# Kernel tuning notes

Measured on AMD Instinct MI355X. Metric: run time of the kernel, lower is better.

## Reference

```python
import jax, jax.numpy as jnp
import numpy as np

H = 16
HD = 128
ROPE_BASE = 10000.0

def _rope_cos_sin(T, dtype):
    inv_freq = 1.0 / (ROPE_BASE ** (jnp.arange(0, HD, 2, dtype=jnp.float32) / HD))  # [HD/2]
    pos = jnp.arange(T, dtype=jnp.float32)
    freqs = pos[:, None] * inv_freq[None, :]  # [T, HD/2]
    return jnp.cos(freqs).astype(dtype), jnp.sin(freqs).astype(dtype)

def _apply_rotary(x, cos, sin):
    # x: [B,H,T,HD]; cos/sin: [T,HD/2]
    x1, x2 = x[..., : HD // 2], x[..., HD // 2 :]
    c = cos[None, None, :, :]
    s = sin[None, None, :, :]
    return jnp.concatenate([x1 * c - x2 * s, x1 * s + x2 * c], axis=-1)

def setup_inputs() -> dict:
    key = jax.random.key(0)
    ks = jax.random.split(key, 5)
    B, T, D = 2, 2048, 2048
    x = jax.random.normal(ks[0], (B, T, D), dtype=jnp.float32)
    Wqkv = jax.random.normal(ks[1], (3 * D, D), dtype=jnp.float32) * (D ** -0.5)
    bqkv = jax.random.normal(ks[2], (3 * D,), dtype=jnp.float32) * 0.02
    Wo = jax.random.normal(ks[3], (D, D), dtype=jnp.float32) * (D ** -0.5)
    bo = jax.random.normal(ks[4], (D,), dtype=jnp.float32) * 0.02
    # causal mask: True = masked (future positions)
    mask = jnp.triu(jnp.ones((T, T), dtype=bool), k=1)[None, None, :, :]
    return {"x": x, "Wqkv": Wqkv, "bqkv": bqkv, "Wo": Wo, "bo": bo, "mask": mask}

def reference(x, Wqkv, bqkv, Wo, bo, mask):
    B, T, D = x.shape
    qkv = x @ Wqkv.T + bqkv  # [B,T,3D]
    q, k, v = jnp.split(qkv, 3, axis=-1)
    def to_heads(t):
        return t.reshape(B, T, H, HD).transpose(0, 2, 1, 3)  # [B,H,T,HD]
    q, k, v = to_heads(q), to_heads(k), to_heads(v)
    cos, sin = _rope_cos_sin(T, x.dtype)
    q = _apply_rotary(q, cos, sin)
    k = _apply_rotary(k, cos, sin)
    scale = HD ** 0.5
    attn = jnp.einsum('bhqd,bhkd->bhqk', q, k) / scale
    neg = -jnp.finfo(x.dtype).max
    attn = jnp.where(mask, neg, attn)
    w = jax.nn.softmax(attn, axis=-1)
    out = jnp.einsum('bhqk,bhkd->bhqd', w, v)  # [B,H,T,HD]
    out = out.transpose(0, 2, 1, 3).reshape(B, T, H * HD)
    return out @ Wo.T + bo
```

## Files before the change

### kernel.cpp

```cpp
#include <hip/hip_runtime.h>
#include <hip/hip_bf16.h>
#include <cstdint>

typedef __bf16 bf16;
typedef __bf16 bf16x8 __attribute__((ext_vector_type(8)));
typedef float  f32x4  __attribute__((ext_vector_type(4)));

#define B_   2
#define T_   2048
#define D_   2048
#define H_   16
#define HD_  128

typedef __attribute__((address_space(3))) void       lds_void;
typedef __attribute__((address_space(1))) const void gbl_void;
__device__ __forceinline__ void glds16(const bf16* g, bf16* l) {
    __builtin_amdgcn_global_load_lds((gbl_void*)g, (lds_void*)l, 16, 0, 0);
}

__device__ __forceinline__ ushort4 cvt4(const float4 v) {
    union { bf16 h[4]; ushort4 u; } pk;
    pk.h[0] = (bf16)v.x; pk.h[1] = (bf16)v.y;
    pk.h[2] = (bf16)v.z; pk.h[3] = (bf16)v.w;
    return pk.u;
}

__global__ __launch_bounds__(256) void convert_xw_kernel(
    const float* __restrict__ x, const float* __restrict__ wqkv,
    bf16* __restrict__ xb, bf16* __restrict__ wqkvb)
{
    const int NX = (B_ * T_ * D_) / 4;
    const int NT = NX + (3 * D_ * D_) / 4;
    for (int g = blockIdx.x * blockDim.x + threadIdx.x; g < NT;
         g += gridDim.x * blockDim.x) {
        if (g < NX) ((ushort4*)xb)[g]      = cvt4(((const float4*)x)[g]);
        else        ((ushort4*)wqkvb)[g-NX] = cvt4(((const float4*)wqkv)[g-NX]);
    }
}

__global__ __launch_bounds__(256) void convert_wo_kernel(
    const float* __restrict__ wo, bf16* __restrict__ wob)
{
    const int N = (D_ * D_) / 4;
    for (int g = blockIdx.x * blockDim.x + threadIdx.x; g < N;
         g += gridDim.x * blockDim.x)
        ((ushort4*)wob)[g] = cvt4(((const float4*)wo)[g]);
}

__device__ __forceinline__ void gemm_core_glds(
    const bf16* __restrict__ A, const bf16* __restrict__ W, int K,
    int bm, int bn, int tid, f32x4 (&acc)[4][4],
    bf16* lds_a, bf16* lds_b)
{
    const int lane = tid & 63, quad = lane >> 4, lcol = lane & 15;
    const int wave = tid >> 6;
    const int wm = (wave >> 1) * 64, wn2 = (wave & 1) * 32;
    const int sw = lcol & 7;
    const int sr = tid >> 3, pc = tid & 7;
    const int sc = (pc ^ (sr & 7)) * 8;
    const bf16* abase = A + (size_t)(bm * 128 + sr) * K + sc;
    const bf16* bbase = W + (size_t)(bn * 128 + sr) * K + sc;
    bf16* la = lds_a + sr * 64 + pc * 8;
    bf16* lb = lds_b + sr * 64 + pc * 8;

    for (int k0 = 0; k0 < K; k0 += 64) {
        __syncthreads();
#pragma unroll
        for (int p = 0; p < 4; p++) {
            glds16(abase + k0 + (size_t)32 * p * K, la + 2048 * p);
            glds16(bbase + k0 + (size_t)32 * p * K, lb + 2048 * p);
        }
        __syncthreads();
#pragma unroll
        for (int kk = 0; kk < 2; kk++) {
            bf16x8 af[4], bfr[4];
#pragma unroll
            for (int i = 0; i < 4; i++)
                af[i] = *(const bf16x8*)&lds_a[(wm + i * 16 + lcol) * 64 +
                                               (((kk * 4 + quad) ^ sw) * 8)];
#pragma unroll
            for (int j = 0; j < 4; j++) {
                const int row = wn2 + (j & 1) * 16 + (j >> 1) * 64 + lcol;
                bfr[j] = *(const bf16x8*)&lds_b[row * 64 +
                                                (((kk * 4 + quad) ^ sw) * 8)];
            }
#pragma unroll
            for (int i = 0; i < 4; i++)
#pragma unroll
                for (int j = 0; j < 4; j++)
                    acc[i][j] = __builtin_amdgcn_mfma_f32_16x16x32_bf16(af[i], bfr[j], acc[i][j], 0, 0, 0);
        }
    }
}

__global__ __launch_bounds__(256) void qkv_gemm_kernel(
    const bf16* __restrict__ xb, const bf16* __restrict__ wqkvb,
    const float* __restrict__ bias,
    bf16* __restrict__ qh, bf16* __restrict__ kh, bf16* __restrict__ vT)
{
    __shared__ bf16 lds_a[128 * 64];
    __shared__ bf16 lds_b[128 * 64];
    const int tid = threadIdx.x;
    const int bm = blockIdx.y, bn = blockIdx.x;
    const int lane = tid & 63, quad = lane >> 4, lcol = lane & 15;
    const int wave = tid >> 6;
    const int wm = (wave >> 1) * 64, wn2 = (wave & 1) * 32;

    f32x4 acc[4][4];
    const f32x4 z = {0.f, 0.f, 0.f, 0.f};
#pragma unroll
    for (int i = 0; i < 4; i++)
#pragma unroll
        for (int j = 0; j < 4; j++) acc[i][j] = z;

    gemm_core_glds(xb, wqkvb, D_, bm, bn, tid, acc, lds_a, lds_b);

    const int n0 = bn * 128;
    const int part = bn / 16;
    const int h = bn & 15;
    const int mb0 = bm * 128 + wm;

    if (part < 2) {
        bf16* dst = (part == 0) ? qh : kh;
#pragma unroll
        for (int i = 0; i < 4; i++) {
#pragma unroll
            for (int jp = 0; jp < 2; jp++) {
                const int d1 = wn2 + jp * 16 + lcol;
                const float invf = __expf(-0.14391156831212787f * (float)d1);
                const float b1 = bias[n0 + d1];
                const float b2 = bias[n0 + d1 + 64];
#pragma unroll
                for (int r = 0; r < 4; r++) {
                    const int m = mb0 + i * 16 + quad * 4 + r;
                    const int bb = m >> 11, t = m & (T_ - 1);
                    const float x1 = acc[i][jp][r] + b1;
                    const float x2 = acc[i][jp + 2][r] + b2;
                    float s, c;
                    __sincosf((float)t * invf, &s, &c);
                    const size_t rowo = ((size_t)(bb * H_ + h) * T_ + t) * HD_;
                    dst[rowo + d1]      = (bf16)(x1 * c - x2 * s);
                    dst[rowo + d1 + 64] = (bf16)(x1 * s + x2 * c);
                }
            }
        }
    } else {
        const int bb = mb0 >> 11, t64 = mb0 & (T_ - 1);
        const int bh = bb * H_ + h;
#pragma unroll
        for (int j = 0; j < 4; j++) {
            const int d = wn2 + (j & 1) * 16 + (j >> 1) * 64 + lcol;
            const float bv = bias[n0 + d];
            bf16* vdst = &vT[((size_t)bh * HD_ + d) * T_ + t64];
#pragma unroll
            for (int r = 0; r < 4; r++) {
                union { bf16 hh[4]; ushort4 u; } pk;
#pragma unroll
                for (int i = 0; i < 4; i++) pk.hh[i] = (bf16)(acc[i][j][r] + bv);
                *(ushort4*)&vdst[(quad * 4 + r) * 4] = pk.u;
            }
        }
    }
}

__global__ __launch_bounds__(256, 4) void attn_kernel(
    const bf16* __restrict__ qh, const bf16* __restrict__ kh,
    const bf16* __restrict__ vT, bf16* __restrict__ ctx)
{
    __shared__ bf16 lds_k[2][64 * 128];
    __shared__ bf16 lds_p[64 * 64];
    const int tid = threadIdx.x;
    const int id = blockIdx.x;
    const int bh = id & 31;
    const int q5 = (id >> 5) & 15;
    const int qt = (id >> 9) ? (31 - q5) : q5;
    const int q0 = qt * 64;
    const int lane = tid & 63, quad = lane >> 4, lcol = lane & 15;
    const int wave = tid >> 6;
    const int wq0 = wave * 16;
    const float scale2 = 0.08838834764831845f * 1.4426950408889634f;

    const bf16* kbase = kh + (size_t)bh * T_ * HD_;
    const bf16* vbase = vT + (size_t)bh * HD_ * T_;

    const int srow = tid >> 4;
    const int scol = ((tid & 15) ^ srow) << 3;
    const bf16* kstage = kbase + (size_t)srow * HD_ + scol;

    bf16x8 qf[4];
#pragma unroll
    for (int kk = 0; kk < 4; kk++)
        qf[kk] = *(const bf16x8*)&qh[((size_t)bh * T_ + q0 + wq0 + lcol) * HD_ +
                                     kk * 32 + quad * 8];

    f32x4 o[8];
    const f32x4 z = {0.f, 0.f, 0.f, 0.f};
#pragma unroll
    for (int jd = 0; jd < 8; jd++) o[jd] = z;
    float l_part[4] = {0.f, 0.f, 0.f, 0.f};

    const int ktmax = qt + 1;
#pragma unroll
    for (int p = 0; p < 4; p++)
        glds16(kstage + (size_t)p * 16 * HD_, &lds_k[0][tid * 8 + p * 2048]);

    for (int kt = 0; kt < ktmax; kt++) {
        __syncthreads();
        if (kt + 1 < ktmax) {
            const bf16* ks = kstage + (size_t)(kt + 1) * 64 * HD_;
#pragma unroll
            for (int p = 0; p < 4; p++)
                glds16(ks + (size_t)p * 16 * HD_,
                       &lds_k[(kt + 1) & 1][tid * 8 + p * 2048]);
        }
        const bf16* lk = lds_k[kt & 1];

        f32x4 s_acc[4];
#pragma unroll
        for (int j = 0; j < 4; j++) s_acc[j] = z;
        __builtin_amdgcn_s_setprio(1);
#pragma unroll
        for (int kk = 0; kk < 4; kk++) {
#pragma unroll
            for (int j = 0; j < 4; j++) {
                const bf16x8 bk = *(const bf16x8*)&lk[(j * 16 + lcol) * 128 +
                                        (((kk * 4 + quad) ^ lcol) << 3)];
                s_acc[j] = __builtin_amdgcn_mfma_f32_16x16x32_bf16(qf[kk], bk, s_acc[j], 0, 0, 0);
            }
        }
        __builtin_amdgcn_s_setprio(0);

        const bool diag = (kt == qt);
#pragma unroll
        for (int r = 0; r < 4; r++) {
            const int prow = wq0 + quad * 4 + r;
            const int qrow = q0 + prow;
            union { bf16 hh[4]; ushort4 u; } pk;
            float lp = 0.f;
#pragma unroll
            for (int j = 0; j < 4; j++) {
                float p = exp2f(fmaf(s_acc[j][r], scale2, -16.0f));
                if (diag) {
                    const int kcol = kt * 64 + j * 16 + lcol;
                    p = (kcol > qrow) ? 0.f : p;
                }
                lp += p;
                pk.hh[j] = (bf16)p;
            }
            l_part[r] += lp;
            *(ushort4*)&lds_p[prow * 64 + ((lcol * 4) ^ ((prow & 7) << 3))] = pk.u;
        }

        const bf16* vrow = vbase + kt * 64 + quad * 8;
#pragma unroll
        for (int kk2 = 0; kk2 < 2; kk2++) {
            const int prow = wq0 + lcol;
            const bf16x8 pf = *(const bf16x8*)&lds_p[prow * 64 +
                                  ((kk2 * 32 + quad * 8) ^ ((lcol & 7) << 3))];
            bf16x8 vf[8];
#pragma unroll
            for (int jd = 0; jd < 8; jd++)
                vf[jd] = *(const bf16x8*)&vrow[(size_t)(jd * 16 + lcol) * T_ + kk2 * 32];
            __builtin_amdgcn_s_setprio(1);
#pragma unroll
            for (int jd = 0; jd < 8; jd++)
                o[jd] = __builtin_amdgcn_mfma_f32_16x16x32_bf16(pf, vf[jd], o[jd], 0, 0, 0);
            __builtin_amdgcn_s_setprio(0);
        }
    }

    float inv_l[4];
#pragma unroll
    for (int r = 0; r < 4; r++) {
        float rs = l_part[r];
#pragma unroll
        for (int off = 1; off < 16; off <<= 1)
            rs += __shfl_xor(rs, off);
        inv_l[r] = 1.0f / rs;
    }
    const int b = bh >> 4, h = bh & 15;
#pragma unroll
    for (int r = 0; r < 4; r++) {
        const int t = q0 + wq0 + quad * 4 + r;
#pragma unroll
        for (int jd = 0; jd < 8; jd++)
            ctx[((size_t)(b * T_ + t)) * D_ + h * HD_ + jd * 16 + lcol] =
                (bf16)(o[jd][r] * inv_l[r]);
    }
}

__global__ __launch_bounds__(256) void proj_gemm_kernel(
    const bf16* __restrict__ ctx, const bf16* __restrict__ wob,
    const float* __restrict__ bias, float* __restrict__ out)
{
    __shared__ bf16 lds_a[128 * 64];
    __shared__ bf16 lds_b[128 * 64];
    const int tid = threadIdx.x;
    const int bm = blockIdx.y, bn = blockIdx.x;
    const int lane = tid & 63, quad = lane >> 4, lcol = lane & 15;
    const int wave = tid >> 6;
    const int wm = (wave >> 1) * 64, wn2 = (wave & 1) * 32;

    f32x4 acc[4][4];
    const f32x4 z = {0.f, 0.f, 0.f, 0.f};
#pragma unroll
    for (int i = 0; i < 4; i++)
#pragma unroll
        for (int j = 0; j < 4; j++) acc[i][j] = z;

    gemm_core_glds(ctx, wob, D_, bm, bn, tid, acc, lds_a, lds_b);

    const int n0 = bn * 128;
#pragma unroll
    for (int i = 0; i < 4; i++) {
#pragma unroll
        for (int j = 0; j < 4; j++) {
            const int n = n0 + wn2 + (j & 1) * 16 + (j >> 1) * 64 + lcol;
            const float bv = bias[n];
#pragma unroll
            for (int r = 0; r < 4; r++) {
                const int m = bm * 128 + wm + i * 16 + quad * 4 + r;
                out[(size_t)m * D_ + n] = acc[i][j][r] + bv;
            }
        }
    }
}

extern "C" void kernel_launch(void* const* d_in, const int* in_sizes, int n_in,
                              void* d_out, int out_size, void* d_ws, size_t ws_size,
                              hipStream_t stream)
{
    const float* x    = (const float*)d_in[0];
    const float* Wqkv = (const float*)d_in[1];
    const float* bqkv = (const float*)d_in[2];
    const float* Wo   = (const float*)d_in[3];
    const float* bo   = (const float*)d_in[4];
    float* out = (float*)d_out;

    const size_t HT = (size_t)B_ * H_ * T_ * HD_;
    bf16* xb   = (bf16*)d_ws;
    bf16* qh   = xb + HT;
    bf16* kh   = qh + HT;
    bf16* vT   = kh + HT;
    bf16* ctx  = xb;
    bf16* wob  = qh;
    bf16* wqkvb = (bf16*)d_out;

    convert_xw_kernel<<<2560, 256, 0, stream>>>(x, Wqkv, xb, wqkvb);
    qkv_gemm_kernel<<<dim3(48, 32), 256, 0, stream>>>(xb, wqkvb, bqkv, qh, kh, vT);
    attn_kernel<<<1024, 256, 0, stream>>>(qh, kh, vT, ctx);
    convert_wo_kernel<<<1024, 256, 0, stream>>>(Wo, wob);
    proj_gemm_kernel<<<dim3(16, 32), 256, 0, stream>>>(ctx, wob, bo, out);
}
```

Measured before the change: 440.1 us.

## Stage V tiles through double-buffered LDS with async global-to-LDS loads

V^T tiles are now prefetched into a swizzled, double-buffered LDS region with global_load_lds, alongside K. Previously each wave read V directly from global memory inside the PV loop. This moves the V load off the critical path and shares it across the four waves. It adds 32KB of LDS per block, and the launch-bounds occupancy hint of 4 is dropped, so occupancy may fall.

```diff
diff --git a/kernel.cpp b/kernel.cpp
--- a/kernel.cpp
+++ b/kernel.cpp
@@ -163,11 +163,12 @@
     }
 }
 
-__global__ __launch_bounds__(256, 4) void attn_kernel(
+__global__ __launch_bounds__(256) void attn_kernel(
     const bf16* __restrict__ qh, const bf16* __restrict__ kh,
     const bf16* __restrict__ vT, bf16* __restrict__ ctx)
 {
     __shared__ bf16 lds_k[2][64 * 128];
+    __shared__ bf16 lds_v[2][128 * 64];
     __shared__ bf16 lds_p[64 * 64];
     const int tid = threadIdx.x;
     const int id = blockIdx.x;
@@ -183,9 +184,10 @@
     const bf16* kbase = kh + (size_t)bh * T_ * HD_;
     const bf16* vbase = vT + (size_t)bh * HD_ * T_;
 
-    const int srow = tid >> 4;
-    const int scol = ((tid & 15) ^ srow) << 3;
-    const bf16* kstage = kbase + (size_t)srow * HD_ + scol;
+    const int ksrow = tid >> 4;
+    const bf16* kstage = kbase + (size_t)ksrow * HD_ + (((tid & 15) ^ ksrow) << 3);
+    const int vsd = tid >> 3;
+    const bf16* vstage = vbase + (size_t)vsd * T_ + (((tid & 7) ^ (vsd & 7)) << 3);
 
     bf16x8 qf[4];
 #pragma unroll
@@ -201,19 +203,26 @@
 
     const int ktmax = qt + 1;
 #pragma unroll
-    for (int p = 0; p < 4; p++)
-        glds16(kstage + (size_t)p * 16 * HD_, &lds_k[0][tid * 8 + p * 2048]);
+    for (int p = 0; p < 4; p++) {
+        glds16(kstage + (size_t)16 * p * HD_, &lds_k[0][tid * 8 + p * 2048]);
+        glds16(vstage + (size_t)32 * p * T_, &lds_v[0][tid * 8 + p * 2048]);
+    }
 
     for (int kt = 0; kt < ktmax; kt++) {
         __syncthreads();
         if (kt + 1 < ktmax) {
             const bf16* ks = kstage + (size_t)(kt + 1) * 64 * HD_;
-#pragma unroll
-            for (int p = 0; p < 4; p++)
-                glds16(ks + (size_t)p * 16 * HD_,
-                       &lds_k[(kt + 1) & 1][tid * 8 + p * 2048]);
+            const bf16* vs = vstage + (kt + 1) * 64;
+            bf16* lkd = &lds_k[(kt + 1) & 1][tid * 8];
+            bf16* lvd = &lds_v[(kt + 1) & 1][tid * 8];
+#pragma unroll
+            for (int p = 0; p < 4; p++) {
+                glds16(ks + (size_t)16 * p * HD_, lkd + p * 2048);
+                glds16(vs + (size_t)32 * p * T_, lvd + p * 2048);
+            }
         }
         const bf16* lk = lds_k[kt & 1];
+        const bf16* lv = lds_v[kt & 1];
 
         f32x4 s_acc[4];
 #pragma unroll
@@ -251,7 +260,6 @@
             *(ushort4*)&lds_p[prow * 64 + ((lcol * 4) ^ ((prow & 7) << 3))] = pk.u;
         }
 
-        const bf16* vrow = vbase + kt * 64 + quad * 8;
 #pragma unroll
         for (int kk2 = 0; kk2 < 2; kk2++) {
             const int prow = wq0 + lcol;
@@ -259,8 +267,11 @@
                                   ((kk2 * 32 + quad * 8) ^ ((lcol & 7) << 3))];
             bf16x8 vf[8];
 #pragma unroll
-            for (int jd = 0; jd < 8; jd++)
-                vf[jd] = *(const bf16x8*)&vrow[(size_t)(jd * 16 + lcol) * T_ + kk2 * 32];
+            for (int jd = 0; jd < 8; jd++) {
+                const int d = jd * 16 + lcol;
+                vf[jd] = *(const bf16x8*)&lv[d * 64 +
+                              (((kk2 * 4 + quad) ^ (lcol & 7)) << 3)];
+            }
             __builtin_amdgcn_s_setprio(1);
 #pragma unroll
             for (int jd = 0; jd < 8; jd++)
```

Measured after the change: 353.5 us (median of 2 runs). -19.7%, faster.
